# Kernel optimization log

Measured on AMD Instinct MI355X. Metric: run time of the kernel, lower is better.

Reference implementation:

```python
import jax, jax.numpy as jnp
import numpy as np

A = 2048        # atoms
IN_DEPTH = 128
OUT_DEPTH = 128
FILTER_LEN = 16


def setup_inputs() -> dict:
    key = jax.random.key(0)
    k1, k2, k3, k4 = jax.random.split(key, 4)
    node_property_tensor = jax.random.normal(k1, (A, IN_DEPTH), dtype=jnp.float32)
    connectivity_tensor = jax.random.normal(k2, (A, A, FILTER_LEN), dtype=jnp.float32)
    bond_property_tensor = jax.random.normal(k3, (A, FILTER_LEN, 2), dtype=jnp.float32)
    # filters initialized ~ N(0,1) * 1/in_depth, per the torch init
    filters = jax.random.normal(k4, (OUT_DEPTH, FILTER_LEN, IN_DEPTH + 2), dtype=jnp.float32) / IN_DEPTH
    return {
        "node_property_tensor": node_property_tensor,
        "connectivity_tensor": connectivity_tensor,
        "bond_property_tensor": bond_property_tensor,
        "filters": filters,
    }


def reference(node_property_tensor, connectivity_tensor, bond_property_tensor, filters):
    # gather neighbor features: conn (A,B,F) x node (B,D) -> (A,F,D)
    node_connection = jnp.einsum('abf,bd->afd', connectivity_tensor, node_property_tensor)
    # append bond properties -> (A, F, D+2)
    combined = jnp.concatenate([node_connection, bond_property_tensor], axis=2)
    # fused broadcast-multiply + double-sum: (A,F,K) x (O,F,K) -> (A,O)
    return jnp.einsum('afk,ofk->ao', combined, filters)
```

## Files before the change

kernel.cpp:

```cpp
#include <hip/hip_runtime.h>
#include <stdint.h>

#define N_ATOM 2048
#define K_TOT  32768
#define NKCH   32
#define KCHUNK 1024
#define BK     64

typedef __attribute__((ext_vector_type(8))) short bf16x8;
typedef __attribute__((ext_vector_type(4))) float f32x4;

typedef __attribute__((address_space(3))) uint32_t lds_u32;
typedef __attribute__((address_space(1))) uint32_t gbl_u32;

__device__ __forceinline__ void async_ld16(const void* g, void* l) {
  __builtin_amdgcn_global_load_lds((const gbl_u32*)g, (lds_u32*)l, 16, 0, 0);
}

__device__ __forceinline__ unsigned short f2bf(float x) {
  union { float f; uint32_t u; } v; v.f = x;
  uint32_t r = v.u + 0x7FFFu + ((v.u >> 16) & 1u);
  return (unsigned short)(r >> 16);
}

__global__ __launch_bounds__(256) void k_gt(const float* __restrict__ node,
                                            const float* __restrict__ filt,
                                            unsigned short* __restrict__ Gt) {
  __shared__ unsigned short As[128 * 136];
  __shared__ unsigned short Bs[128 * 136];
  const int t  = threadIdx.x;
  const int b0 = blockIdx.x * 128;
  const int n0 = blockIdx.y * 128;

#pragma unroll
  for (int rep = 0; rep < 16; ++rep) {
    int q = rep * 256 + t;
    int row = q >> 5, c4 = q & 31;
    float4 v = *(const float4*)(node + (size_t)(b0 + row) * 128 + c4 * 4);
    unsigned short* dst = &As[row * 136 + c4 * 4];
    dst[0] = f2bf(v.x); dst[1] = f2bf(v.y); dst[2] = f2bf(v.z); dst[3] = f2bf(v.w);
  }
#pragma unroll
  for (int rep = 0; rep < 32; ++rep) {
    int q = rep * 256 + t;
    int row = q >> 6, c2 = q & 63;
    float2 v = *(const float2*)(filt + (size_t)(n0 + row) * 130 + c2 * 2);
    unsigned short* dst = &Bs[row * 136 + c2 * 2];
    dst[0] = f2bf(v.x); dst[1] = f2bf(v.y);
  }
  __syncthreads();

  const int w = t >> 6, l = t & 63;
  const int lm = l & 15, q4 = l >> 4;

  f32x4 acc[2][8];
#pragma unroll
  for (int ms = 0; ms < 2; ++ms)
#pragma unroll
    for (int ns = 0; ns < 8; ++ns)
      acc[ms][ns] = (f32x4){0.f, 0.f, 0.f, 0.f};

#pragma unroll
  for (int ks = 0; ks < 4; ++ks) {
    int ko = ks * 32 + q4 * 8;
    bf16x8 a[2], b[8];
#pragma unroll
    for (int ms = 0; ms < 2; ++ms) {
      int m = w * 32 + ms * 16 + lm;
      a[ms] = *(const bf16x8*)&As[m * 136 + ko];
    }
#pragma unroll
    for (int ns = 0; ns < 8; ++ns) {
      int n = ns * 16 + lm;
      b[ns] = *(const bf16x8*)&Bs[n * 136 + ko];
    }
#pragma unroll
    for (int ms = 0; ms < 2; ++ms)
#pragma unroll
      for (int ns = 0; ns < 8; ++ns)
        acc[ms][ns] = __builtin_amdgcn_mfma_f32_16x16x32_bf16(a[ms], b[ns], acc[ms][ns], 0, 0, 0);
  }

#pragma unroll
  for (int ms = 0; ms < 2; ++ms)
#pragma unroll
    for (int ns = 0; ns < 8; ++ns)
#pragma unroll
      for (int i = 0; i < 4; ++i) {
        int m = w * 32 + ms * 16 + q4 * 4 + i;
        int n = ns * 16 + lm;
        Gt[(size_t)(b0 + m) * 2048 + n0 + n] = f2bf(acc[ms][ns][i]);
      }
}

__global__ __launch_bounds__(128) void k_bond(const float* __restrict__ bond,
                                              const float* __restrict__ filt,
                                              float* __restrict__ out) {
  __shared__ float bl[32];
  const int a = blockIdx.x, t = threadIdx.x;
  if (t < 32) bl[t] = bond[a * 32 + t];
  __syncthreads();
  float acc = 0.f;
  const float* fp = filt + (size_t)t * 2080 + 128;
#pragma unroll
  for (int f = 0; f < 16; ++f)
    acc += bl[2 * f] * fp[f * 130] + bl[2 * f + 1] * fp[f * 130 + 1];
  out[(size_t)a * 128 + t] = acc;
}

__global__ __launch_bounds__(256) void k_main(const float* __restrict__ conn,
                                              const unsigned short* __restrict__ Gt,
                                              float* __restrict__ out) {
  __shared__ float Af[128 * BK];
  __shared__ unsigned short Bh[(BK / 16) * 128 * 16];

  const int t  = threadIdx.x;
  const int w  = t >> 6, l = t & 63;
  const int lm = l & 15, q4 = l >> 4;
  const int a0 = blockIdx.x * 128;
  const int kc = blockIdx.y * KCHUNK;

  f32x4 acc[2][8];
#pragma unroll
  for (int ms = 0; ms < 2; ++ms)
#pragma unroll
    for (int ns = 0; ns < 8; ++ns)
      acc[ms][ns] = (f32x4){0.f, 0.f, 0.f, 0.f};

  const float4* Af4 = (const float4*)Af;

  for (int it = 0; it < KCHUNK / BK; ++it) {
    const int k0 = kc + it * BK;
    __syncthreads();

    {
      const int mt = t >> 4, cp = t & 15;
#pragma unroll
      for (int r = 0; r < 8; ++r) {
        int m = r * 16 + mt;
        int c = cp ^ (m & 15);
        const float* g = conn + (size_t)(a0 + m) * K_TOT + k0 + c * 4;
        void* lb = (void*)((char*)Af + r * 4096 + w * 1024);
        async_ld16(g, lb);
      }
    }
    {
      const unsigned short* gB = Gt + (size_t)k0 * 128;
#pragma unroll
      for (int r = 0; r < 4; ++r) {
        const void* g = gB + (size_t)(r * 256 + t) * 8;
        void* lb = (void*)((char*)Bh + r * 4096 + w * 1024);
        async_ld16(g, lb);
      }
    }
    __syncthreads();

#pragma unroll
    for (int kk = 0; kk < 2; ++kk) {
      const int b_rel = 2 * kk + (q4 >> 1);
      const int f0 = (q4 & 1) * 8;
      bf16x8 b[8];
#pragma unroll
      for (int ns = 0; ns < 8; ++ns) {
        int o = ns * 16 + lm;
        b[ns] = *(const bf16x8*)&Bh[b_rel * 2048 + o * 16 + f0];
      }
      const int c0 = kk * 8 + q4 * 2;
      bf16x8 a[2];
#pragma unroll
      for (int ms = 0; ms < 2; ++ms) {
        int m = w * 32 + ms * 16 + lm;
        float4 lo = Af4[m * 16 + (c0 ^ (m & 15))];
        float4 hi = Af4[m * 16 + ((c0 + 1) ^ (m & 15))];
        bf16x8 av;
        av[0] = (short)f2bf(lo.x); av[1] = (short)f2bf(lo.y);
        av[2] = (short)f2bf(lo.z); av[3] = (short)f2bf(lo.w);
        av[4] = (short)f2bf(hi.x); av[5] = (short)f2bf(hi.y);
        av[6] = (short)f2bf(hi.z); av[7] = (short)f2bf(hi.w);
        a[ms] = av;
      }
#pragma unroll
      for (int ms = 0; ms < 2; ++ms)
#pragma unroll
        for (int ns = 0; ns < 8; ++ns)
          acc[ms][ns] = __builtin_amdgcn_mfma_f32_16x16x32_bf16(a[ms], b[ns], acc[ms][ns], 0, 0, 0);
    }
  }

#pragma unroll
  for (int ms = 0; ms < 2; ++ms)
#pragma unroll
    for (int ns = 0; ns < 8; ++ns)
#pragma unroll
      for (int i = 0; i < 4; ++i) {
        int m = w * 32 + ms * 16 + q4 * 4 + i;
        int n = ns * 16 + lm;
        atomicAdd(&out[(size_t)(a0 + m) * 128 + n], acc[ms][ns][i]);
      }
}

extern "C" void kernel_launch(void* const* d_in, const int* in_sizes, int n_in,
                              void* d_out, int out_size, void* d_ws, size_t ws_size,
                              hipStream_t stream) {
  const float* node = (const float*)d_in[0];
  const float* conn = (const float*)d_in[1];
  const float* bond = (const float*)d_in[2];
  const float* filt = (const float*)d_in[3];
  float* out = (float*)d_out;

  if (ws_size < (size_t)N_ATOM * 2048 * sizeof(unsigned short)) return;
  unsigned short* Gt = (unsigned short*)d_ws;

  k_gt  <<<dim3(16, 16), 256, 0, stream>>>(node, filt, Gt);
  k_bond<<<dim3(2048),   128, 0, stream>>>(bond, filt, out);
  k_main<<<dim3(16, 32), 256, 0, stream>>>(conn, Gt, out);
}
```

Baseline: 425.4 us.

## Load conn directly to registers and double-buffer Gt tiles in main GEMM

The main kernel stops staging the fp32 connectivity tile through LDS. Each lane now loads its A fragments straight from global memory into registers. Gt tiles are double-buffered in LDS, so the next tile's loads are issued before the current tile's MFMAs, and there is one barrier per iteration. The K chunk grows to 2048, which halves the grid to 256 blocks and halves the atomic adds on the output, and the bond kernel is batched 16 atoms per block with the filters staged in LDS. The risks are higher register pressure from the prefetched fp32 A values, fewer blocks to spread across the CUs, and direct global loads that may coalesce worse than the async LDS loads.

```diff
diff --git a/kernel.cpp b/kernel.cpp
--- a/kernel.cpp
+++ b/kernel.cpp
@@ -3,9 +3,9 @@
 
 #define N_ATOM 2048
 #define K_TOT  32768
-#define NKCH   32
-#define KCHUNK 1024
-#define BK     64
+#define KCH    2048
+#define BK2    128
+#define NIT    (KCH / BK2)
 
 typedef __attribute__((ext_vector_type(8))) short bf16x8;
 typedef __attribute__((ext_vector_type(4))) float f32x4;
@@ -93,32 +93,51 @@
       }
 }
 
-__global__ __launch_bounds__(128) void k_bond(const float* __restrict__ bond,
+__global__ __launch_bounds__(256) void k_bond(const float* __restrict__ bond,
                                               const float* __restrict__ filt,
                                               float* __restrict__ out) {
-  __shared__ float bl[32];
-  const int a = blockIdx.x, t = threadIdx.x;
-  if (t < 32) bl[t] = bond[a * 32 + t];
+  __shared__ float fb[128 * 32];
+  __shared__ float bl[16 * 32];
+  const int t  = threadIdx.x;
+  const int a0 = blockIdx.x * 16;
+
+#pragma unroll
+  for (int r = 0; r < 16; ++r) {
+    int idx = r * 256 + t;
+    int o = idx >> 5, fj = idx & 31;
+    int f = fj >> 1, j = fj & 1;
+    fb[idx] = filt[(size_t)o * 2080 + f * 130 + 128 + j];
+  }
+  bl[t]       = bond[(size_t)a0 * 32 + t];
+  bl[256 + t] = bond[(size_t)a0 * 32 + 256 + t];
   __syncthreads();
-  float acc = 0.f;
-  const float* fp = filt + (size_t)t * 2080 + 128;
-#pragma unroll
-  for (int f = 0; f < 16; ++f)
-    acc += bl[2 * f] * fp[f * 130] + bl[2 * f + 1] * fp[f * 130 + 1];
-  out[(size_t)a * 128 + t] = acc;
-}
-
-__global__ __launch_bounds__(256) void k_main(const float* __restrict__ conn,
-                                              const unsigned short* __restrict__ Gt,
-                                              float* __restrict__ out) {
-  __shared__ float Af[128 * BK];
-  __shared__ unsigned short Bh[(BK / 16) * 128 * 16];
+
+#pragma unroll
+  for (int r = 0; r < 8; ++r) {
+    int idx = r * 256 + t;
+    int aa = idx >> 7, o = idx & 127;
+    const float2* bp = (const float2*)&bl[aa * 32];
+    const float2* fp = (const float2*)&fb[o * 32];
+    float acc = 0.f;
+#pragma unroll
+    for (int f = 0; f < 16; ++f) {
+      float2 b2 = bp[f], f2 = fp[f];
+      acc += b2.x * f2.x + b2.y * f2.y;
+    }
+    out[(size_t)(a0 + aa) * 128 + o] = acc;
+  }
+}
+
+__global__ __launch_bounds__(256, 1) void k_main(const float* __restrict__ conn,
+                                                 const unsigned short* __restrict__ Gt,
+                                                 float* __restrict__ out) {
+  __shared__ unsigned short Bh[2][8 * 128 * 16];
 
   const int t  = threadIdx.x;
   const int w  = t >> 6, l = t & 63;
   const int lm = l & 15, q4 = l >> 4;
   const int a0 = blockIdx.x * 128;
-  const int kc = blockIdx.y * KCHUNK;
+  const int kc = blockIdx.y * KCH;
 
   f32x4 acc[2][8];
 #pragma unroll
@@ -127,64 +146,75 @@
     for (int ns = 0; ns < 8; ++ns)
       acc[ms][ns] = (f32x4){0.f, 0.f, 0.f, 0.f};
 
-  const float4* Af4 = (const float4*)Af;
-
-  for (int it = 0; it < KCHUNK / BK; ++it) {
-    const int k0 = kc + it * BK;
-    __syncthreads();
-
-    {
-      const int mt = t >> 4, cp = t & 15;
-#pragma unroll
-      for (int r = 0; r < 8; ++r) {
-        int m = r * 16 + mt;
-        int c = cp ^ (m & 15);
-        const float* g = conn + (size_t)(a0 + m) * K_TOT + k0 + c * 4;
-        void* lb = (void*)((char*)Af + r * 4096 + w * 1024);
-        async_ld16(g, lb);
-      }
-    }
-    {
-      const unsigned short* gB = Gt + (size_t)k0 * 128;
-#pragma unroll
-      for (int r = 0; r < 4; ++r) {
-        const void* g = gB + (size_t)(r * 256 + t) * 8;
-        void* lb = (void*)((char*)Bh + r * 4096 + w * 1024);
-        async_ld16(g, lb);
-      }
-    }
-    __syncthreads();
-
-#pragma unroll
-    for (int kk = 0; kk < 2; ++kk) {
-      const int b_rel = 2 * kk + (q4 >> 1);
-      const int f0 = (q4 & 1) * 8;
-      bf16x8 b[8];
-#pragma unroll
-      for (int ns = 0; ns < 8; ++ns) {
-        int o = ns * 16 + lm;
-        b[ns] = *(const bf16x8*)&Bh[b_rel * 2048 + o * 16 + f0];
-      }
-      const int c0 = kk * 8 + q4 * 2;
-      bf16x8 a[2];
-#pragma unroll
-      for (int ms = 0; ms < 2; ++ms) {
-        int m = w * 32 + ms * 16 + lm;
-        float4 lo = Af4[m * 16 + (c0 ^ (m & 15))];
-        float4 hi = Af4[m * 16 + ((c0 + 1) ^ (m & 15))];
+  const float* arow0 = conn + (size_t)(a0 + w * 32 + lm) * K_TOT;
+  const float* arow1 = conn + (size_t)(a0 + w * 32 + 16 + lm) * K_TOT;
+
+  auto stageB = [&](int buf, int k0) {
+    const char* gB = (const char*)(Gt + (size_t)k0 * 128);
+#pragma unroll
+    for (int r = 0; r < 8; ++r) {
+      const void* g = gB + (size_t)(r * 256 + t) * 16;
+      void* lb = (void*)((char*)&Bh[buf][0] + r * 4096 + w * 1024);
+      async_ld16(g, lb);
+    }
+  };
+
+  float4 Ar[2][4][2];
+  auto loadA = [&](int k0) {
+#pragma unroll
+    for (int kk = 0; kk < 4; ++kk) {
+      int off = k0 + kk * 32 + q4 * 8;
+      Ar[0][kk][0] = *(const float4*)(arow0 + off);
+      Ar[0][kk][1] = *(const float4*)(arow0 + off + 4);
+      Ar[1][kk][0] = *(const float4*)(arow1 + off);
+      Ar[1][kk][1] = *(const float4*)(arow1 + off + 4);
+    }
+  };
+
+  stageB(0, kc);
+  loadA(kc);
+  __syncthreads();
+
+  for (int it = 0; it < NIT; ++it) {
+    const int cur = it & 1;
+
+    bf16x8 af[2][4];
+#pragma unroll
+    for (int ms = 0; ms < 2; ++ms)
+#pragma unroll
+      for (int kk = 0; kk < 4; ++kk) {
+        float4 lo = Ar[ms][kk][0], hi = Ar[ms][kk][1];
         bf16x8 av;
         av[0] = (short)f2bf(lo.x); av[1] = (short)f2bf(lo.y);
         av[2] = (short)f2bf(lo.z); av[3] = (short)f2bf(lo.w);
         av[4] = (short)f2bf(hi.x); av[5] = (short)f2bf(hi.y);
         av[6] = (short)f2bf(hi.z); av[7] = (short)f2bf(hi.w);
-        a[ms] = av;
+        af[ms][kk] = av;
+      }
+
+    if (it + 1 < NIT) {
+      stageB(1 - cur, kc + (it + 1) * BK2);
+      loadA(kc + (it + 1) * BK2);
+    }
+
+#pragma unroll
+    for (int kk = 0; kk < 4; ++kk) {
+      const int b_rel = 2 * kk + (q4 >> 1);
+      const int f0 = (q4 & 1) * 8;
+      bf16x8 b[8];
+#pragma unroll
+      for (int ns = 0; ns < 8; ++ns) {
+        int o = ns * 16 + lm;
+        b[ns] = *(const bf16x8*)&Bh[cur][b_rel * 2048 + o * 16 + f0];
       }
 #pragma unroll
       for (int ms = 0; ms < 2; ++ms)
 #pragma unroll
         for (int ns = 0; ns < 8; ++ns)
-          acc[ms][ns] = __builtin_amdgcn_mfma_f32_16x16x32_bf16(a[ms], b[ns], acc[ms][ns], 0, 0, 0);
-    }
+          acc[ms][ns] = __builtin_amdgcn_mfma_f32_16x16x32_bf16(af[ms][kk], b[ns], acc[ms][ns], 0, 0, 0);
+    }
+
+    __syncthreads();
   }
 
 #pragma unroll
@@ -212,6 +242,6 @@
   unsigned short* Gt = (unsigned short*)d_ws;
 
   k_gt  <<<dim3(16, 16), 256, 0, stream>>>(node, filt, Gt);
-  k_bond<<<dim3(2048),   128, 0, stream>>>(bond, filt, out);
-  k_main<<<dim3(16, 32), 256, 0, stream>>>(conn, Gt, out);
-}
+  k_bond<<<dim3(128),    256, 0, stream>>>(bond, filt, out);
+  k_main<<<dim3(16, 16), 256, 0, stream>>>(conn, Gt, out);
+}
```

New measurement: 430.0 us. Within noise of the previous version (+1.1%).
